# Performance work log

Hardware: AMD Instinct MI355X
Metric: run time of the kernel (lower is better)

Reference implementation:

```python
import jax, jax.numpy as jnp
import numpy as np

I_T = 0.5      # IoU threshold
EPS = 1e-07    # FocalLoss eps
GAMMA = 2.0    # FocalLoss gamma
C_IN = 500
N_CLS = 3


def _box_iou(boxes):
    # boxes: (P, 4) in xyxy -> pairwise IoU (P, P), matching torchvision.ops.box_iou
    area = (boxes[:, 2] - boxes[:, 0]) * (boxes[:, 3] - boxes[:, 1])
    lt = jnp.maximum(boxes[:, None, :2], boxes[None, :, :2])
    rb = jnp.minimum(boxes[:, None, 2:], boxes[None, :, 2:])
    wh = jnp.clip(rb - lt, 0.0)
    inter = wh[..., 0] * wh[..., 1]
    return inter / (area[:, None] + area[None, :] - inter)


def setup_inputs() -> dict:
    key = jax.random.key(0)
    k1, k2, k3, k4, k5, k6, k7 = jax.random.split(key, 7)
    bs, P = 16, 2048
    inputs = jax.random.normal(k1, (bs * P, C_IN), jnp.float32)
    pre_score = jax.random.uniform(k2, (bs, P, N_CLS), jnp.float32)
    labels = jax.random.randint(k3, (bs, N_CLS), 0, 2).astype(bool)
    # valid xyxy boxes in a ~512x512 image
    xy1 = jax.random.uniform(k4, (bs, P, 2), jnp.float32) * 400.0
    wh = jax.random.uniform(k5, (bs, P, 2), jnp.float32) * 104.0 + 8.0
    rois = jnp.concatenate([xy1, xy1 + wh], axis=-1)
    fc_w = jax.random.normal(k6, (4, C_IN), jnp.float32) * (1.0 / np.sqrt(C_IN))
    fc_b = jax.random.normal(k7, (4,), jnp.float32) * 0.01
    return {"inputs": inputs, "pre_score": pre_score, "labels": labels,
            "rois": rois, "num": 2048, "fc_w": fc_w, "fc_b": fc_b}


def reference(inputs, pre_score, labels, rois, num, fc_w, fc_b):
    bs = pre_score.shape[0]
    P = num
    dt = inputs.dtype

    # fc + softmax over class dim
    xr_k = jax.nn.softmax((inputs @ fc_w.T + fc_b).reshape(bs, P, 4), axis=2)

    # pairwise IoU per batch: (bs, P, P)
    iou = jax.vmap(_box_iou)(rois)

    # candidate seed proposals: score > 0.5; fallback to single argmax when <= 1 candidate
    cand = pre_score > 0.5                                   # (bs, P, 3)
    ncand = cand.sum(axis=1, keepdims=True)                  # (bs, 1, 3)
    fb = jax.nn.one_hot(jnp.argmax(pre_score, axis=1), P, axis=1, dtype=bool)  # (bs, P, 3)
    cand = jnp.where(ncand <= 1, fb, cand)
    lab = labels.astype(bool)

    # sequential (c = 0,1,2) strict-greater argmax assignment, as in the torch loops
    I = jnp.zeros((bs, P), dt)
    w = jnp.zeros((bs, P), dt)
    hits = []
    for c in range(N_CLS):
        m = jnp.where(cand[:, None, :, c], iou, -1.0)        # mask non-candidate columns
        best = m.max(axis=-1)                                # (bs, P)
        jstar = m.argmax(axis=-1)                            # first-max tie-break, as torch
        xbest = jnp.take_along_axis(pre_score[:, :, c], jstar, axis=1)
        best = jnp.where(lab[:, c:c + 1], best, -1.0)        # class skipped if label off
        upd = best > I
        w = jnp.where(upd, xbest, w)
        hits.append(upd & (best > I_T))
        I = jnp.where(upd, best, I)
    h = jnp.stack(hits, axis=-1)                             # (bs, P, 3)
    y_k = jnp.concatenate([h.astype(dt),
                           (~h.any(axis=-1, keepdims=True)).astype(dt)], axis=-1)
    target = jnp.argmax(y_k.reshape(bs * P, 4), axis=1)      # first class with y==1, else 3

    # FocalLoss(gamma=2) applied to already-softmaxed scores (double softmax, as original)
    logit = jnp.clip(jax.nn.softmax(xr_k.reshape(bs * P, 4), axis=1), EPS, 1.0 - EPS)
    pt = jnp.take_along_axis(logit, target[:, None], axis=1)[:, 0]
    floss = -jnp.log(pt) * (1.0 - pt) ** GAMMA               # (N,)

    # original computes mean(w.view(N,1) * loss(N,)) which broadcasts to (N,N);
    # that equals mean(w) * mean(loss) -- computed without materializing N^2.
    loss = jnp.mean(w.reshape(-1)) * jnp.mean(floss)
    return (xr_k, loss)
```

## Files before the change

kernel.cpp:

```cpp
#include <hip/hip_runtime.h>
#include <math.h>

#define BS   16
#define PP   2048
#define CIN  500
#define NROW (BS * PP)
#define JQ   256
#define NQ   8
#define IT   256
#define NIT  8
#define NBLK_IOU (BS * NIT * NQ)
#define NBT2 (BS * NIT)
#define HIMASK 0xFFFFF800u

__global__ void __launch_bounds__(256) fc_softmax_kernel(
    const float* __restrict__ inputs, const float* __restrict__ fc_w,
    const float* __restrict__ fc_b, float* __restrict__ out)
{
    __shared__ float4 wL[CIN];
    int tid = threadIdx.x;
    for (int k = tid; k < CIN; k += 256)
        wL[k] = make_float4(fc_w[k], fc_w[CIN + k], fc_w[2 * CIN + k], fc_w[3 * CIN + k]);
    __syncthreads();

    int lane = tid & 63;
    int wv   = tid >> 6;
#pragma unroll
    for (int r = 0; r < 4; ++r) {
        int row = blockIdx.x * 16 + wv * 4 + r;
        const float4* in4 = (const float4*)(inputs + (size_t)row * CIN);
        float a0 = 0.f, a1 = 0.f, a2 = 0.f, a3 = 0.f;
#pragma unroll
        for (int t = 0; t < 2; ++t) {
            int f = t * 64 + lane;
            if (f < 125) {
                float4 x = in4[f];
                float4 w0 = wL[f * 4 + 0], w1 = wL[f * 4 + 1];
                float4 w2 = wL[f * 4 + 2], w3 = wL[f * 4 + 3];
                a0 += x.x * w0.x + x.y * w1.x + x.z * w2.x + x.w * w3.x;
                a1 += x.x * w0.y + x.y * w1.y + x.z * w2.y + x.w * w3.y;
                a2 += x.x * w0.z + x.y * w1.z + x.z * w2.z + x.w * w3.z;
                a3 += x.x * w0.w + x.y * w1.w + x.z * w2.w + x.w * w3.w;
            }
        }
#pragma unroll
        for (int off = 32; off > 0; off >>= 1) {
            a0 += __shfl_xor(a0, off);
            a1 += __shfl_xor(a1, off);
            a2 += __shfl_xor(a2, off);
            a3 += __shfl_xor(a3, off);
        }
        if (lane == 0) {
            a0 += fc_b[0]; a1 += fc_b[1]; a2 += fc_b[2]; a3 += fc_b[3];
            float m = fmaxf(fmaxf(a0, a1), fmaxf(a2, a3));
            float e0 = expf(a0 - m), e1 = expf(a1 - m), e2 = expf(a2 - m), e3 = expf(a3 - m);
            float inv = 1.0f / (e0 + e1 + e2 + e3);
            ((float4*)out)[row] = make_float4(e0 * inv, e1 * inv, e2 * inv, e3 * inv);
        }
    }
}

__global__ void __launch_bounds__(256) prep_kernel(
    const float* __restrict__ pre_score, const float* __restrict__ rois,
    uint4* __restrict__ mrec)
{
    int b = blockIdx.x;
    int tid = threadIdx.x;
    __shared__ float sv[256];
    __shared__ int   si[256];
    __shared__ int   sc[256];

    float v0[8], v1[8], v2[8];
    unsigned char bits[8];
#pragma unroll
    for (int t = 0; t < 8; ++t) {
        int j = t * 256 + tid;
        const float* p = pre_score + ((size_t)b * PP + j) * 3;
        v0[t] = p[0]; v1[t] = p[1]; v2[t] = p[2];
        bits[t] = 0;
    }

#define PREP_CLASS(VV, CBIT)                                                   \
    {                                                                          \
        float bv = -1.0f; int bi = 0; int cnt = 0;                             \
        _Pragma("unroll")                                                      \
        for (int t = 0; t < 8; ++t) {                                          \
            int j = t * 256 + tid;                                             \
            float v = VV[t];                                                   \
            if (v > 0.5f) cnt++;                                               \
            if (v > bv) { bv = v; bi = j; }                                    \
        }                                                                      \
        sv[tid] = bv; si[tid] = bi; sc[tid] = cnt;                             \
        __syncthreads();                                                       \
        for (int s2 = 128; s2 > 0; s2 >>= 1) {                                 \
            if (tid < s2) {                                                    \
                float ov = sv[tid + s2]; int oi = si[tid + s2];                \
                if (ov > sv[tid] || (ov == sv[tid] && oi < si[tid])) {         \
                    sv[tid] = ov; si[tid] = oi;                                \
                }                                                              \
                sc[tid] += sc[tid + s2];                                       \
            }                                                                  \
            __syncthreads();                                                   \
        }                                                                      \
        int total = sc[0];                                                     \
        int amax  = si[0];                                                     \
        __syncthreads();                                                       \
        _Pragma("unroll")                                                      \
        for (int t = 0; t < 8; ++t) {                                          \
            int j = t * 256 + tid;                                             \
            bool cb = (total <= 1) ? (j == amax) : (VV[t] > 0.5f);             \
            if (cb) bits[t] |= (unsigned char)(CBIT);                          \
        }                                                                      \
    }

    PREP_CLASS(v0, 1)
    PREP_CLASS(v1, 2)
    PREP_CLASS(v2, 4)
#undef PREP_CLASS

    const float4* rb = (const float4*)(rois + (size_t)b * PP * 4);
#pragma unroll
    for (int t = 0; t < 8; ++t) {
        int j = t * 256 + tid;
        float4 bx = rb[j];
        float area = (bx.z - bx.x) * (bx.w - bx.y);
        uint4 r;
        r.x = __float_as_uint(area);
        r.y = (bits[t] & 1) ? 0xFFFFFFFFu : 0u;
        r.z = (bits[t] & 2) ? 0xFFFFFFFFu : 0u;
        r.w = (bits[t] & 4) ? 0xFFFFFFFFu : 0u;
        mrec[(size_t)b * PP + j] = r;
    }
}

__global__ void __launch_bounds__(512) iou_kernel(
    const float* __restrict__ rois, const uint4* __restrict__ mrec,
    unsigned* __restrict__ qres)
{
    __shared__ float4   boxesL[JQ];
    __shared__ uint4    mrecL[JQ];
    __shared__ unsigned bestA[3][8][IT];
    int bid = blockIdx.x;
    int q   = bid & 7;
    int it  = (bid >> 3) & 7;
    int b   = bid >> 6;
    int tid = threadIdx.x;

    const float4* rbase = (const float4*)(rois + (size_t)b * PP * 4);
    if (tid < JQ) boxesL[tid] = rbase[q * JQ + tid];
    else          mrecL[tid - JQ] = mrec[(size_t)b * PP + q * JQ + (tid - JQ)];
    __syncthreads();

    int lane = tid & 63, w = tid >> 6;
    float4 bx[4];
    float  ax[4];
#pragma unroll
    for (int s = 0; s < 4; ++s) {
        bx[s] = rbase[it * IT + s * 64 + lane];
        ax[s] = (bx[s].z - bx[s].x) * (bx[s].w - bx[s].y);
    }

    int jb = w * 32;
    int jfbase = 2047 - q * JQ - jb;

    unsigned best[4][3];
#pragma unroll
    for (int s = 0; s < 4; ++s) {
        best[s][0] = 0u; best[s][1] = 0u; best[s][2] = 0u;
    }

#pragma unroll 4
    for (int jj = 0; jj < 32; ++jj) {
        float4 bj = boxesL[jb + jj];
        uint4  mj = mrecL[jb + jj];
        float  aj = __uint_as_float(mj.x);
        unsigned jf = (unsigned)(jfbase - jj);
#pragma unroll
        for (int s = 0; s < 4; ++s) {
            float lx = fmaxf(bx[s].x, bj.x), ly = fmaxf(bx[s].y, bj.y);
            float rx = fminf(bx[s].z, bj.z), ry = fminf(bx[s].w, bj.w);
            float ww = fmaxf(rx - lx, 0.f), hh = fmaxf(ry - ly, 0.f);
            float inter = ww * hh;
            float uni   = ax[s] + aj - inter;
            float iou   = inter * __builtin_amdgcn_rcpf(uni);
            unsigned pk = (__float_as_uint(iou) & HIMASK) | jf;
            unsigned k0 = pk & mj.y, k1 = pk & mj.z, k2 = pk & mj.w;
            best[s][0] = best[s][0] > k0 ? best[s][0] : k0;
            best[s][1] = best[s][1] > k1 ? best[s][1] : k1;
            best[s][2] = best[s][2] > k2 ? best[s][2] : k2;
        }
    }
#pragma unroll
    for (int s = 0; s < 4; ++s) {
        bestA[0][w][s * 64 + lane] = best[s][0];
        bestA[1][w][s * 64 + lane] = best[s][1];
        bestA[2][w][s * 64 + lane] = best[s][2];
    }
    __syncthreads();

    if (tid < IT) {
#pragma unroll
        for (int c = 0; c < 3; ++c) {
            unsigned m = bestA[c][0][tid];
#pragma unroll
            for (int w2 = 1; w2 < 8; ++w2) {
                unsigned o = bestA[c][w2][tid];
                m = m > o ? m : o;
            }
            qres[(((size_t)b * NQ + q) * 3 + c) * PP + it * IT + tid] = m;
        }
    }
}

__global__ void __launch_bounds__(256) merge_focal_kernel(
    const unsigned* __restrict__ qres, const float* __restrict__ pre_score,
    const int* __restrict__ labels, const float* __restrict__ xr,
    float* __restrict__ partials)
{
    __shared__ float redw[4], redf[4];
    int bt = blockIdx.x;
    int b = bt >> 3, it = bt & 7;
    int tid = threadIdx.x;
    int i = it * IT + tid;

    float I = 0.f, wv = 0.f;
    int target = 3;
#pragma unroll
    for (int c = 0; c < 3; ++c) {
        unsigned k = 0u;
#pragma unroll
        for (int qq = 0; qq < NQ; ++qq) {
            unsigned h = qres[(((size_t)b * NQ + qq) * 3 + c) * PP + i];
            k = k > h ? k : h;
        }
        int   jv    = 2047 - (int)(k & 2047u);
        float bestv = __uint_as_float(k & HIMASK);
        bestv = (labels[b * 3 + c] != 0) ? bestv : -1.0f;
        if (bestv > I) {
            wv = pre_score[((size_t)b * PP + jv) * 3 + c];
            if (bestv > 0.5f && target == 3) target = c;
            I = bestv;
        }
    }
    int gi = b * PP + i;
    float4 x4 = ((const float4*)xr)[gi];
    float m = fmaxf(fmaxf(x4.x, x4.y), fmaxf(x4.z, x4.w));
    float e0 = expf(x4.x - m), e1 = expf(x4.y - m), e2 = expf(x4.z - m), e3 = expf(x4.w - m);
    float ssum = e0 + e1 + e2 + e3;
    float et = (target == 0) ? e0 : (target == 1) ? e1 : (target == 2) ? e2 : e3;
    float pt = et / ssum;
    pt = fminf(fmaxf(pt, 1e-7f), 1.0f - 1e-7f);
    float fl = -logf(pt) * (1.0f - pt) * (1.0f - pt);

    float sw = wv, sf = fl;
#pragma unroll
    for (int off = 32; off > 0; off >>= 1) {
        sw += __shfl_down(sw, off);
        sf += __shfl_down(sf, off);
    }
    if ((tid & 63) == 0) { redw[tid >> 6] = sw; redf[tid >> 6] = sf; }
    __syncthreads();
    if (tid == 0) {
        partials[bt * 2 + 0] = redw[0] + redw[1] + redw[2] + redw[3];
        partials[bt * 2 + 1] = redf[0] + redf[1] + redf[2] + redf[3];
    }
}

__global__ void __launch_bounds__(256) finalize_kernel(
    const float* __restrict__ partials, float* __restrict__ out_loss)
{
    __shared__ float swL[256], sfL[256];
    int tid = threadIdx.x;
    float sw = (tid < NBT2) ? partials[2 * tid] : 0.f;
    float sf = (tid < NBT2) ? partials[2 * tid + 1] : 0.f;
    swL[tid] = sw; sfL[tid] = sf;
    __syncthreads();
    for (int s = 128; s > 0; s >>= 1) {
        if (tid < s) { swL[tid] += swL[tid + s]; sfL[tid] += sfL[tid + s]; }
        __syncthreads();
    }
    if (tid == 0)
        out_loss[0] = (swL[0] / (float)NROW) * (sfL[0] / (float)NROW);
}

extern "C" void kernel_launch(void* const* d_in, const int* in_sizes, int n_in,
                              void* d_out, int out_size, void* d_ws, size_t ws_size,
                              hipStream_t stream)
{
    const float* inputs    = (const float*)d_in[0];
    const float* pre_score = (const float*)d_in[1];
    const int*   labels    = (const int*)d_in[2];
    const float* rois      = (const float*)d_in[3];
    const float* fc_w      = (const float*)d_in[5];
    const float* fc_b      = (const float*)d_in[6];

    float* out = (float*)d_out;
    unsigned* qres = (unsigned*)d_ws;
    uint4* mrec = (uint4*)((char*)d_ws
                 + (size_t)BS * NQ * 3 * PP * sizeof(unsigned));
    float* partials = (float*)((char*)mrec + (size_t)BS * PP * sizeof(uint4));

    prep_kernel<<<BS, 256, 0, stream>>>(pre_score, rois, mrec);
    fc_softmax_kernel<<<NROW / 16, 256, 0, stream>>>(inputs, fc_w, fc_b, out);
    iou_kernel<<<NBLK_IOU, 512, 0, stream>>>(rois, mrec, qres);
    merge_focal_kernel<<<NBT2, 256, 0, stream>>>(qres, pre_score, labels, out, partials);
    finalize_kernel<<<1, 256, 0, stream>>>(partials, out + (size_t)NROW * 4);
}
```

Before: 70.40 us.

## Stream IoU column records via scalar loads and fold finalize into merge kernel

The prep kernel now writes a packed 32-byte record per box (coordinates, area, three class masks). The IoU kernel drops its LDS staging and per-iteration LDS reads. Each wave instead fetches its wave-uniform column record with s_load_dwordx8 through inline asm, double-buffered against the compute. The separate finalize kernel is replaced by a last-block-done atomic counter inside merge_focal, which saves one launch at the cost of a memset and threadfences.

```diff
diff --git a/kernel.cpp b/kernel.cpp
--- a/kernel.cpp
+++ b/kernel.cpp
@@ -13,6 +13,8 @@
 #define NBT2 (BS * NIT)
 #define HIMASK 0xFFFFF800u
 
+typedef int v8i __attribute__((ext_vector_type(8)));
+
 __global__ void __launch_bounds__(256) fc_softmax_kernel(
     const float* __restrict__ inputs, const float* __restrict__ fc_w,
     const float* __restrict__ fc_b, float* __restrict__ out)
@@ -62,7 +64,7 @@
 
 __global__ void __launch_bounds__(256) prep_kernel(
     const float* __restrict__ pre_score, const float* __restrict__ rois,
-    uint4* __restrict__ mrec)
+    uint4* __restrict__ rec2)
 {
     int b = blockIdx.x;
     int tid = threadIdx.x;
@@ -124,34 +126,33 @@
         int j = t * 256 + tid;
         float4 bx = rb[j];
         float area = (bx.z - bx.x) * (bx.w - bx.y);
-        uint4 r;
-        r.x = __float_as_uint(area);
-        r.y = (bits[t] & 1) ? 0xFFFFFFFFu : 0u;
-        r.z = (bits[t] & 2) ? 0xFFFFFFFFu : 0u;
-        r.w = (bits[t] & 4) ? 0xFFFFFFFFu : 0u;
-        mrec[(size_t)b * PP + j] = r;
+        uint4 lo, hi;
+        lo.x = __float_as_uint(bx.x);
+        lo.y = __float_as_uint(bx.y);
+        lo.z = __float_as_uint(bx.z);
+        lo.w = __float_as_uint(bx.w);
+        hi.x = __float_as_uint(area);
+        hi.y = (bits[t] & 1) ? 0xFFFFFFFFu : 0u;
+        hi.z = (bits[t] & 2) ? 0xFFFFFFFFu : 0u;
+        hi.w = (bits[t] & 4) ? 0xFFFFFFFFu : 0u;
+        rec2[((size_t)b * PP + j) * 2 + 0] = lo;
+        rec2[((size_t)b * PP + j) * 2 + 1] = hi;
     }
 }
 
 __global__ void __launch_bounds__(512) iou_kernel(
-    const float* __restrict__ rois, const uint4* __restrict__ mrec,
+    const float* __restrict__ rois, const uint4* __restrict__ rec2,
     unsigned* __restrict__ qres)
 {
-    __shared__ float4   boxesL[JQ];
-    __shared__ uint4    mrecL[JQ];
     __shared__ unsigned bestA[3][8][IT];
     int bid = blockIdx.x;
     int q   = bid & 7;
     int it  = (bid >> 3) & 7;
     int b   = bid >> 6;
     int tid = threadIdx.x;
+    int lane = tid & 63, w = tid >> 6;
 
     const float4* rbase = (const float4*)(rois + (size_t)b * PP * 4);
-    if (tid < JQ) boxesL[tid] = rbase[q * JQ + tid];
-    else          mrecL[tid - JQ] = mrec[(size_t)b * PP + q * JQ + (tid - JQ)];
-    __syncthreads();
-
-    int lane = tid & 63, w = tid >> 6;
     float4 bx[4];
     float  ax[4];
 #pragma unroll
@@ -160,36 +161,57 @@
         ax[s] = (bx[s].z - bx[s].x) * (bx[s].w - bx[s].y);
     }
 
-    int jb = w * 32;
-    int jfbase = 2047 - q * JQ - jb;
+    int jb  = w * 32;
+    unsigned off = (unsigned)(((b * PP) + q * JQ + jb) * 32);
+    off = __builtin_amdgcn_readfirstlane(off);
+    unsigned long long addr = (unsigned long long)rec2 + off;
+    int jfbase = 2047 - (q * JQ + (int)__builtin_amdgcn_readfirstlane(jb));
 
     unsigned best[4][3];
 #pragma unroll
-    for (int s = 0; s < 4; ++s) {
-        best[s][0] = 0u; best[s][1] = 0u; best[s][2] = 0u;
-    }
+    for (int s = 0; s < 4; ++s) { best[s][0] = 0u; best[s][1] = 0u; best[s][2] = 0u; }
+
+    v8i cur, nxt;
+    asm volatile("s_load_dwordx8 %0, %1, 0x0" : "=&s"(cur) : "s"(addr));
+    asm volatile("s_waitcnt lgkmcnt(0)" : "+s"(cur));
 
 #pragma unroll 4
     for (int jj = 0; jj < 32; ++jj) {
-        float4 bj = boxesL[jb + jj];
-        uint4  mj = mrecL[jb + jj];
-        float  aj = __uint_as_float(mj.x);
-        unsigned jf = (unsigned)(jfbase - jj);
-#pragma unroll
-        for (int s = 0; s < 4; ++s) {
-            float lx = fmaxf(bx[s].x, bj.x), ly = fmaxf(bx[s].y, bj.y);
-            float rx = fminf(bx[s].z, bj.z), ry = fminf(bx[s].w, bj.w);
-            float ww = fmaxf(rx - lx, 0.f), hh = fmaxf(ry - ly, 0.f);
-            float inter = ww * hh;
-            float uni   = ax[s] + aj - inter;
-            float iou   = inter * __builtin_amdgcn_rcpf(uni);
-            unsigned pk = (__float_as_uint(iou) & HIMASK) | jf;
-            unsigned k0 = pk & mj.y, k1 = pk & mj.z, k2 = pk & mj.w;
-            best[s][0] = best[s][0] > k0 ? best[s][0] : k0;
-            best[s][1] = best[s][1] > k1 ? best[s][1] : k1;
-            best[s][2] = best[s][2] > k2 ? best[s][2] : k2;
-        }
-    }
+        if (jj < 31) {
+            addr += 32;
+            asm volatile("s_load_dwordx8 %0, %1, 0x0" : "=&s"(nxt) : "s"(addr));
+        }
+        {
+            float bjx = __uint_as_float((unsigned)cur[0]);
+            float bjy = __uint_as_float((unsigned)cur[1]);
+            float bjz = __uint_as_float((unsigned)cur[2]);
+            float bjw = __uint_as_float((unsigned)cur[3]);
+            float aj  = __uint_as_float((unsigned)cur[4]);
+            unsigned m0 = (unsigned)cur[5];
+            unsigned m1 = (unsigned)cur[6];
+            unsigned m2 = (unsigned)cur[7];
+            unsigned jf = (unsigned)(jfbase - jj);
+#pragma unroll
+            for (int s = 0; s < 4; ++s) {
+                float lx = fmaxf(bx[s].x, bjx), ly = fmaxf(bx[s].y, bjy);
+                float rx = fminf(bx[s].z, bjz), ry = fminf(bx[s].w, bjw);
+                float ww = fmaxf(rx - lx, 0.f), hh = fmaxf(ry - ly, 0.f);
+                float inter = ww * hh;
+                float uni   = ax[s] + aj - inter;
+                float iou   = inter * __builtin_amdgcn_rcpf(uni);
+                unsigned pk = (__float_as_uint(iou) & HIMASK) | jf;
+                unsigned k0 = pk & m0, k1 = pk & m1, k2 = pk & m2;
+                best[s][0] = best[s][0] > k0 ? best[s][0] : k0;
+                best[s][1] = best[s][1] > k1 ? best[s][1] : k1;
+                best[s][2] = best[s][2] > k2 ? best[s][2] : k2;
+            }
+        }
+        if (jj < 31) {
+            asm volatile("s_waitcnt lgkmcnt(0)" : "+s"(nxt));
+            cur = nxt;
+        }
+    }
+
 #pragma unroll
     for (int s = 0; s < 4; ++s) {
         bestA[0][w][s * 64 + lane] = best[s][0];
@@ -215,9 +237,11 @@
 __global__ void __launch_bounds__(256) merge_focal_kernel(
     const unsigned* __restrict__ qres, const float* __restrict__ pre_score,
     const int* __restrict__ labels, const float* __restrict__ xr,
-    float* __restrict__ partials)
+    float* __restrict__ partials, unsigned* __restrict__ counter,
+    float* __restrict__ out_loss)
 {
     __shared__ float redw[4], redf[4];
+    __shared__ int lastflag;
     int bt = blockIdx.x;
     int b = bt >> 3, it = bt & 7;
     int tid = threadIdx.x;
@@ -263,24 +287,25 @@
     if (tid == 0) {
         partials[bt * 2 + 0] = redw[0] + redw[1] + redw[2] + redw[3];
         partials[bt * 2 + 1] = redf[0] + redf[1] + redf[2] + redf[3];
-    }
-}
-
-__global__ void __launch_bounds__(256) finalize_kernel(
-    const float* __restrict__ partials, float* __restrict__ out_loss)
-{
-    __shared__ float swL[256], sfL[256];
-    int tid = threadIdx.x;
-    float sw = (tid < NBT2) ? partials[2 * tid] : 0.f;
-    float sf = (tid < NBT2) ? partials[2 * tid + 1] : 0.f;
-    swL[tid] = sw; sfL[tid] = sf;
+        __threadfence();
+        unsigned done = atomicAdd(counter, 1u);
+        lastflag = (done == (unsigned)(NBT2 - 1));
+    }
     __syncthreads();
-    for (int s = 128; s > 0; s >>= 1) {
-        if (tid < s) { swL[tid] += swL[tid + s]; sfL[tid] += sfL[tid + s]; }
+    if (lastflag) {
+        __threadfence();
+        __shared__ float swL[256], sfL[256];
+        float asw = (tid < NBT2) ? partials[2 * tid] : 0.f;
+        float asf = (tid < NBT2) ? partials[2 * tid + 1] : 0.f;
+        swL[tid] = asw; sfL[tid] = asf;
         __syncthreads();
-    }
-    if (tid == 0)
-        out_loss[0] = (swL[0] / (float)NROW) * (sfL[0] / (float)NROW);
+        for (int s = 128; s > 0; s >>= 1) {
+            if (tid < s) { swL[tid] += swL[tid + s]; sfL[tid] += sfL[tid + s]; }
+            __syncthreads();
+        }
+        if (tid == 0)
+            out_loss[0] = (swL[0] / (float)NROW) * (sfL[0] / (float)NROW);
+    }
 }
 
 extern "C" void kernel_launch(void* const* d_in, const int* in_sizes, int n_in,
@@ -295,14 +320,17 @@
     const float* fc_b      = (const float*)d_in[6];
 
     float* out = (float*)d_out;
-    unsigned* qres = (unsigned*)d_ws;
-    uint4* mrec = (uint4*)((char*)d_ws
-                 + (size_t)BS * NQ * 3 * PP * sizeof(unsigned));
-    float* partials = (float*)((char*)mrec + (size_t)BS * PP * sizeof(uint4));
-
-    prep_kernel<<<BS, 256, 0, stream>>>(pre_score, rois, mrec);
+    char* ws = (char*)d_ws;
+    unsigned* qres   = (unsigned*)ws;
+    uint4*    rec2   = (uint4*)(ws + 3145728);
+    float*    partials = (float*)(ws + 4194304);
+    unsigned* counter  = (unsigned*)(ws + 4195328);
+
+    hipMemsetAsync(counter, 0, 4, stream);
+    prep_kernel<<<BS, 256, 0, stream>>>(pre_score, rois, rec2);
     fc_softmax_kernel<<<NROW / 16, 256, 0, stream>>>(inputs, fc_w, fc_b, out);
-    iou_kernel<<<NBLK_IOU, 512, 0, stream>>>(rois, mrec, qres);
-    merge_focal_kernel<<<NBT2, 256, 0, stream>>>(qres, pre_score, labels, out, partials);
-    finalize_kernel<<<1, 256, 0, stream>>>(partials, out + (size_t)NROW * 4);
-}
+    iou_kernel<<<NBLK_IOU, 512, 0, stream>>>(rois, rec2, qres);
+    merge_focal_kernel<<<NBT2, 256, 0, stream>>>(qres, pre_score, labels, out,
+                                                 partials, counter,
+                                                 out + (size_t)NROW * 4);
+}
```

New measurement: 80.26 us. 14.0% more time.

## Fuse fc-softmax into IoU kernel and stream j-boxes via scalar loads

Applied to the files above, without the earlier changes.

Merges the fc+softmax kernel into the IoU kernel so each IoU block also handles 32 rows of the linear layer, removing one launch and overlapping the two workloads. The prep kernel now writes a packed 32-byte record per box (coordinates, area, class masks). The IoU inner loop reads these records with double-buffered s_load_dwordx8 scalar loads written in inline asm, instead of staging them in LDS behind a barrier. This relies on wave-uniform addressing and on hand-placed waitcnt and sched_barrier calls. It also raises per-block LDS use because the fc weights are staged there.

```diff
diff --git a/kernel.cpp b/kernel.cpp
--- a/kernel.cpp
+++ b/kernel.cpp
@@ -10,59 +10,14 @@
 #define IT   256
 #define NIT  8
 #define NBLK_IOU (BS * NIT * NQ)
-#define NBT2 (BS * NIT)
+#define NBT2 128
 #define HIMASK 0xFFFFF800u
 
-__global__ void __launch_bounds__(256) fc_softmax_kernel(
-    const float* __restrict__ inputs, const float* __restrict__ fc_w,
-    const float* __restrict__ fc_b, float* __restrict__ out)
-{
-    __shared__ float4 wL[CIN];
-    int tid = threadIdx.x;
-    for (int k = tid; k < CIN; k += 256)
-        wL[k] = make_float4(fc_w[k], fc_w[CIN + k], fc_w[2 * CIN + k], fc_w[3 * CIN + k]);
-    __syncthreads();
-
-    int lane = tid & 63;
-    int wv   = tid >> 6;
-#pragma unroll
-    for (int r = 0; r < 4; ++r) {
-        int row = blockIdx.x * 16 + wv * 4 + r;
-        const float4* in4 = (const float4*)(inputs + (size_t)row * CIN);
-        float a0 = 0.f, a1 = 0.f, a2 = 0.f, a3 = 0.f;
-#pragma unroll
-        for (int t = 0; t < 2; ++t) {
-            int f = t * 64 + lane;
-            if (f < 125) {
-                float4 x = in4[f];
-                float4 w0 = wL[f * 4 + 0], w1 = wL[f * 4 + 1];
-                float4 w2 = wL[f * 4 + 2], w3 = wL[f * 4 + 3];
-                a0 += x.x * w0.x + x.y * w1.x + x.z * w2.x + x.w * w3.x;
-                a1 += x.x * w0.y + x.y * w1.y + x.z * w2.y + x.w * w3.y;
-                a2 += x.x * w0.z + x.y * w1.z + x.z * w2.z + x.w * w3.z;
-                a3 += x.x * w0.w + x.y * w1.w + x.z * w2.w + x.w * w3.w;
-            }
-        }
-#pragma unroll
-        for (int off = 32; off > 0; off >>= 1) {
-            a0 += __shfl_xor(a0, off);
-            a1 += __shfl_xor(a1, off);
-            a2 += __shfl_xor(a2, off);
-            a3 += __shfl_xor(a3, off);
-        }
-        if (lane == 0) {
-            a0 += fc_b[0]; a1 += fc_b[1]; a2 += fc_b[2]; a3 += fc_b[3];
-            float m = fmaxf(fmaxf(a0, a1), fmaxf(a2, a3));
-            float e0 = expf(a0 - m), e1 = expf(a1 - m), e2 = expf(a2 - m), e3 = expf(a3 - m);
-            float inv = 1.0f / (e0 + e1 + e2 + e3);
-            ((float4*)out)[row] = make_float4(e0 * inv, e1 * inv, e2 * inv, e3 * inv);
-        }
-    }
-}
+typedef int v8i __attribute__((ext_vector_type(8)));
 
 __global__ void __launch_bounds__(256) prep_kernel(
     const float* __restrict__ pre_score, const float* __restrict__ rois,
-    uint4* __restrict__ mrec)
+    uint4* __restrict__ rec2)
 {
     int b = blockIdx.x;
     int tid = threadIdx.x;
@@ -124,34 +79,40 @@
         int j = t * 256 + tid;
         float4 bx = rb[j];
         float area = (bx.z - bx.x) * (bx.w - bx.y);
-        uint4 r;
-        r.x = __float_as_uint(area);
-        r.y = (bits[t] & 1) ? 0xFFFFFFFFu : 0u;
-        r.z = (bits[t] & 2) ? 0xFFFFFFFFu : 0u;
-        r.w = (bits[t] & 4) ? 0xFFFFFFFFu : 0u;
-        mrec[(size_t)b * PP + j] = r;
-    }
-}
-
-__global__ void __launch_bounds__(512) iou_kernel(
-    const float* __restrict__ rois, const uint4* __restrict__ mrec,
-    unsigned* __restrict__ qres)
-{
-    __shared__ float4   boxesL[JQ];
-    __shared__ uint4    mrecL[JQ];
+        uint4 lo, hi;
+        lo.x = __float_as_uint(bx.x);
+        lo.y = __float_as_uint(bx.y);
+        lo.z = __float_as_uint(bx.z);
+        lo.w = __float_as_uint(bx.w);
+        hi.x = __float_as_uint(area);
+        hi.y = (bits[t] & 1) ? 0xFFFFFFFFu : 0u;
+        hi.z = (bits[t] & 2) ? 0xFFFFFFFFu : 0u;
+        hi.w = (bits[t] & 4) ? 0xFFFFFFFFu : 0u;
+        rec2[((size_t)b * PP + j) * 2 + 0] = lo;
+        rec2[((size_t)b * PP + j) * 2 + 1] = hi;
+    }
+}
+
+__global__ void __launch_bounds__(512) fused_kernel(
+    const float* __restrict__ rois, const unsigned* __restrict__ rec2d,
+    unsigned* __restrict__ qres,
+    const float* __restrict__ inputs, const float* __restrict__ fc_w,
+    const float* __restrict__ fc_b, float* __restrict__ out)
+{
     __shared__ unsigned bestA[3][8][IT];
+    __shared__ float4   wLf[CIN];
     int bid = blockIdx.x;
     int q   = bid & 7;
     int it  = (bid >> 3) & 7;
     int b   = bid >> 6;
-    int tid = threadIdx.x;
+    int tid = threadIdx.x, lane = tid & 63;
+    int w   = __builtin_amdgcn_readfirstlane(tid >> 6);
+
+    for (int k2 = tid; k2 < CIN; k2 += 512)
+        wLf[k2] = make_float4(fc_w[k2], fc_w[CIN + k2],
+                              fc_w[2 * CIN + k2], fc_w[3 * CIN + k2]);
 
     const float4* rbase = (const float4*)(rois + (size_t)b * PP * 4);
-    if (tid < JQ) boxesL[tid] = rbase[q * JQ + tid];
-    else          mrecL[tid - JQ] = mrec[(size_t)b * PP + q * JQ + (tid - JQ)];
-    __syncthreads();
-
-    int lane = tid & 63, w = tid >> 6;
     float4 bx[4];
     float  ax[4];
 #pragma unroll
@@ -160,36 +121,71 @@
         ax[s] = (bx[s].z - bx[s].x) * (bx[s].w - bx[s].y);
     }
 
-    int jb = w * 32;
-    int jfbase = 2047 - q * JQ - jb;
+    int jb  = q * JQ + w * 32;
+    int jfb = 2047 - jb;
+    unsigned long long addr = (unsigned long long)rec2d
+                            + (unsigned long long)(b * PP + jb) * 32ull;
 
     unsigned best[4][3];
 #pragma unroll
-    for (int s = 0; s < 4; ++s) {
-        best[s][0] = 0u; best[s][1] = 0u; best[s][2] = 0u;
-    }
-
-#pragma unroll 4
-    for (int jj = 0; jj < 32; ++jj) {
-        float4 bj = boxesL[jb + jj];
-        uint4  mj = mrecL[jb + jj];
-        float  aj = __uint_as_float(mj.x);
-        unsigned jf = (unsigned)(jfbase - jj);
-#pragma unroll
-        for (int s = 0; s < 4; ++s) {
-            float lx = fmaxf(bx[s].x, bj.x), ly = fmaxf(bx[s].y, bj.y);
-            float rx = fminf(bx[s].z, bj.z), ry = fminf(bx[s].w, bj.w);
-            float ww = fmaxf(rx - lx, 0.f), hh = fmaxf(ry - ly, 0.f);
-            float inter = ww * hh;
-            float uni   = ax[s] + aj - inter;
-            float iou   = inter * __builtin_amdgcn_rcpf(uni);
-            unsigned pk = (__float_as_uint(iou) & HIMASK) | jf;
-            unsigned k0 = pk & mj.y, k1 = pk & mj.z, k2 = pk & mj.w;
-            best[s][0] = best[s][0] > k0 ? best[s][0] : k0;
-            best[s][1] = best[s][1] > k1 ? best[s][1] : k1;
-            best[s][2] = best[s][2] > k2 ? best[s][2] : k2;
-        }
-    }
+    for (int s = 0; s < 4; ++s) { best[s][0] = 0u; best[s][1] = 0u; best[s][2] = 0u; }
+
+    v8i A0, A1, A2, A3, B0, B1, B2, B3;
+
+#define ISSUE4(R0, R1, R2, R3)                                                 \
+    asm volatile("s_load_dwordx8 %0, %1, 0x0"  : "=&s"(R0) : "s"(addr));       \
+    asm volatile("s_load_dwordx8 %0, %1, 0x20" : "=&s"(R1) : "s"(addr));       \
+    asm volatile("s_load_dwordx8 %0, %1, 0x40" : "=&s"(R2) : "s"(addr));       \
+    asm volatile("s_load_dwordx8 %0, %1, 0x60" : "=&s"(R3) : "s"(addr));       \
+    addr += 128;
+
+#define DO_J(R, KOFF)                                                          \
+    {                                                                          \
+        float bjx = __uint_as_float((unsigned)R[0]);                           \
+        float bjy = __uint_as_float((unsigned)R[1]);                           \
+        float bjz = __uint_as_float((unsigned)R[2]);                           \
+        float bjw = __uint_as_float((unsigned)R[3]);                           \
+        float aj  = __uint_as_float((unsigned)R[4]);                           \
+        unsigned m0 = (unsigned)R[5], m1 = (unsigned)R[6], m2 = (unsigned)R[7];\
+        unsigned jf = (unsigned)(jfb - (KOFF));                                \
+        _Pragma("unroll")                                                      \
+        for (int s = 0; s < 4; ++s) {                                          \
+            float lx = fmaxf(bx[s].x, bjx), ly = fmaxf(bx[s].y, bjy);          \
+            float rx = fminf(bx[s].z, bjz), ry = fminf(bx[s].w, bjw);          \
+            float ww = fmaxf(rx - lx, 0.f), hh = fmaxf(ry - ly, 0.f);          \
+            float inter = ww * hh;                                             \
+            float uni   = (ax[s] + aj) - inter;                                \
+            float iou   = inter * __builtin_amdgcn_rcpf(uni);                  \
+            unsigned pk = (__float_as_uint(iou) & HIMASK) | jf;                \
+            unsigned k0 = pk & m0, k1 = pk & m1, k2 = pk & m2;                 \
+            best[s][0] = best[s][0] > k0 ? best[s][0] : k0;                    \
+            best[s][1] = best[s][1] > k1 ? best[s][1] : k1;                    \
+            best[s][2] = best[s][2] > k2 ? best[s][2] : k2;                    \
+        }                                                                      \
+    }
+
+#define BATCH(C0, C1, C2, C3, N0, N1, N2, N3, BASE, DOISSUE)                   \
+    asm volatile("s_waitcnt lgkmcnt(0)"                                        \
+                 : "+s"(C0), "+s"(C1), "+s"(C2), "+s"(C3));                    \
+    __builtin_amdgcn_sched_barrier(0);                                         \
+    if (DOISSUE) { ISSUE4(N0, N1, N2, N3) }                                    \
+    DO_J(C0, (BASE) + 0) DO_J(C1, (BASE) + 1)                                  \
+    DO_J(C2, (BASE) + 2) DO_J(C3, (BASE) + 3)
+
+    ISSUE4(A0, A1, A2, A3)
+    BATCH(A0, A1, A2, A3, B0, B1, B2, B3,  0, 1)
+    BATCH(B0, B1, B2, B3, A0, A1, A2, A3,  4, 1)
+    BATCH(A0, A1, A2, A3, B0, B1, B2, B3,  8, 1)
+    BATCH(B0, B1, B2, B3, A0, A1, A2, A3, 12, 1)
+    BATCH(A0, A1, A2, A3, B0, B1, B2, B3, 16, 1)
+    BATCH(B0, B1, B2, B3, A0, A1, A2, A3, 20, 1)
+    BATCH(A0, A1, A2, A3, B0, B1, B2, B3, 24, 1)
+    BATCH(B0, B1, B2, B3, A0, A1, A2, A3, 28, 0)
+
+#undef BATCH
+#undef DO_J
+#undef ISSUE4
+
 #pragma unroll
     for (int s = 0; s < 4; ++s) {
         bestA[0][w][s * 64 + lane] = best[s][0];
@@ -208,6 +204,41 @@
                 m = m > o ? m : o;
             }
             qres[(((size_t)b * NQ + q) * 3 + c) * PP + it * IT + tid] = m;
+        }
+    }
+
+#pragma unroll
+    for (int r = 0; r < 4; ++r) {
+        int row = bid * 32 + w * 4 + r;
+        const float4* in4 = (const float4*)(inputs + (size_t)row * CIN);
+        float a0 = 0.f, a1 = 0.f, a2 = 0.f, a3 = 0.f;
+#pragma unroll
+        for (int t = 0; t < 2; ++t) {
+            int f = t * 64 + lane;
+            if (f < 125) {
+                float4 x = in4[f];
+                float4 w0 = wLf[f * 4 + 0], w1 = wLf[f * 4 + 1];
+                float4 w2 = wLf[f * 4 + 2], w3 = wLf[f * 4 + 3];
+                a0 += x.x * w0.x + x.y * w1.x + x.z * w2.x + x.w * w3.x;
+                a1 += x.x * w0.y + x.y * w1.y + x.z * w2.y + x.w * w3.y;
+                a2 += x.x * w0.z + x.y * w1.z + x.z * w2.z + x.w * w3.z;
+                a3 += x.x * w0.w + x.y * w1.w + x.z * w2.w + x.w * w3.w;
+            }
+        }
+#pragma unroll
+        for (int off = 32; off > 0; off >>= 1) {
+            a0 += __shfl_xor(a0, off);
+            a1 += __shfl_xor(a1, off);
+            a2 += __shfl_xor(a2, off);
+            a3 += __shfl_xor(a3, off);
+        }
+        if (lane == 0) {
+            a0 += fc_b[0]; a1 += fc_b[1]; a2 += fc_b[2]; a3 += fc_b[3];
+            float m = fmaxf(fmaxf(a0, a1), fmaxf(a2, a3));
+            float e0 = expf(a0 - m), e1 = expf(a1 - m);
+            float e2 = expf(a2 - m), e3 = expf(a3 - m);
+            float inv = 1.0f / (e0 + e1 + e2 + e3);
+            ((float4*)out)[row] = make_float4(e0 * inv, e1 * inv, e2 * inv, e3 * inv);
         }
     }
 }
@@ -295,14 +326,14 @@
     const float* fc_b      = (const float*)d_in[6];
 
     float* out = (float*)d_out;
-    unsigned* qres = (unsigned*)d_ws;
-    uint4* mrec = (uint4*)((char*)d_ws
-                 + (size_t)BS * NQ * 3 * PP * sizeof(unsigned));
-    float* partials = (float*)((char*)mrec + (size_t)BS * PP * sizeof(uint4));
-
-    prep_kernel<<<BS, 256, 0, stream>>>(pre_score, rois, mrec);
-    fc_softmax_kernel<<<NROW / 16, 256, 0, stream>>>(inputs, fc_w, fc_b, out);
-    iou_kernel<<<NBLK_IOU, 512, 0, stream>>>(rois, mrec, qres);
+    char* ws = (char*)d_ws;
+    unsigned* qres     = (unsigned*)ws;
+    uint4*    rec2     = (uint4*)(ws + 3145728);
+    float*    partials = (float*)(ws + 3145728 + 1048576);
+
+    prep_kernel<<<BS, 256, 0, stream>>>(pre_score, rois, rec2);
+    fused_kernel<<<NBLK_IOU, 512, 0, stream>>>(rois, (const unsigned*)rec2, qres,
+                                               inputs, fc_w, fc_b, out);
     merge_focal_kernel<<<NBT2, 256, 0, stream>>>(qres, pre_score, labels, out, partials);
     finalize_kernel<<<1, 256, 0, stream>>>(partials, out + (size_t)NROW * 4);
 }
```

After: 62.29 us. -11.5%, faster.
